# Kernel optimization log

Hardware: AMD Instinct MI355X
Metric: run time of the kernel (lower is better)

Reference implementation:

```python
import jax, jax.numpy as jnp
import numpy as np

# hyper_params (mode='test')
PRE_NMS = 1000
POST_NMS = 300
IOU_TH = 0.7
VARIANCES = np.array([0.1, 0.1, 0.2, 0.2], dtype=np.float32)
FM = 64            # feature map height/width
ANCHOR_COUNT = 9   # 3 scales x 3 ratios


def _make_anchors():
    """Normalized [y1,x1,y2,x2] anchors on a FM x FM grid, 9 per cell."""
    scales = np.array([0.1, 0.2, 0.4], np.float32)
    ratios = np.array([0.5, 1.0, 2.0], np.float32)
    ws = (scales[:, None] * np.sqrt(ratios)[None, :]).reshape(-1)  # (9,)
    hs = (scales[:, None] / np.sqrt(ratios)[None, :]).reshape(-1)  # (9,)
    ctr = (np.arange(FM, dtype=np.float32) + 0.5) / FM
    cy, cx = np.meshgrid(ctr, ctr, indexing='ij')                  # (FM,FM)
    cy = cy[..., None]; cx = cx[..., None]                         # (FM,FM,1)
    anchors = np.stack([cy - 0.5 * hs, cx - 0.5 * ws,
                        cy + 0.5 * hs, cx + 0.5 * ws], axis=-1)    # (FM,FM,9,4)
    return jnp.asarray(anchors.reshape(-1, 4))                     # (36864,4)


def setup_inputs() -> dict:
    key = jax.random.key(0)
    k1, k2 = jax.random.split(key)
    B = 16
    rpn_bbox_deltas = jax.random.normal(k1, (B, FM, FM, ANCHOR_COUNT * 4), dtype=jnp.float32)
    rpn_labels = jax.random.uniform(k2, (B, FM, FM, ANCHOR_COUNT), dtype=jnp.float32)
    return {"rpn_bbox_deltas": rpn_bbox_deltas,
            "rpn_labels": rpn_labels,
            "anchors": _make_anchors()}


def _nms_single(boxes):
    """Greedy NMS on score-sorted boxes (N,4) -> (POST_NMS,4), zero-padded."""
    N = boxes.shape[0]
    y1, x1, y2, x2 = boxes[:, 0], boxes[:, 1], boxes[:, 2], boxes[:, 3]
    area = (y2 - y1) * (x2 - x1)                                   # (N,)
    iy1 = jnp.maximum(y1[:, None], y1[None, :])
    ix1 = jnp.maximum(x1[:, None], x1[None, :])
    iy2 = jnp.minimum(y2[:, None], y2[None, :])
    ix2 = jnp.minimum(x2[:, None], x2[None, :])
    inter = jnp.maximum(iy2 - iy1, 0.0) * jnp.maximum(ix2 - ix1, 0.0)
    iou = inter / jnp.maximum(area[:, None] + area[None, :] - inter, 1e-9)  # (N,N)
    idx = jnp.arange(N)

    def body(i, keep):
        # if box i survives, suppress later boxes with high overlap
        suppress = keep[i] & (iou[i] > IOU_TH) & (idx > i)
        return keep & ~suppress

    keep = jax.lax.fori_loop(0, N, body, jnp.ones((N,), dtype=bool))
    # stable sort: kept boxes first, original (score-descending) order preserved
    order = jnp.argsort(jnp.where(keep, 0, 1))[:POST_NMS]
    sel = boxes[order]
    valid = keep[order]
    # combined_non_max_suppression clips output boxes to [0,1] and zero-pads
    return jnp.where(valid[:, None], jnp.clip(sel, 0.0, 1.0), 0.0)


def reference(rpn_bbox_deltas, rpn_labels, anchors):
    B = rpn_bbox_deltas.shape[0]
    N = anchors.shape[0]
    deltas = rpn_bbox_deltas.reshape(B, N, 4) * jnp.asarray(VARIANCES)
    labels = rpn_labels.reshape(B, N)

    # decode deltas against anchors
    anc_h = anchors[:, 2] - anchors[:, 0]
    anc_w = anchors[:, 3] - anchors[:, 1]
    anc_cy = anchors[:, 0] + 0.5 * anc_h
    anc_cx = anchors[:, 1] + 0.5 * anc_w
    h = jnp.exp(deltas[..., 2]) * anc_h
    w = jnp.exp(deltas[..., 3]) * anc_w
    cy = deltas[..., 0] * anc_h + anc_cy
    cx = deltas[..., 1] * anc_w + anc_cx
    boxes = jnp.stack([cy - 0.5 * h, cx - 0.5 * w,
                       cy + 0.5 * h, cx + 0.5 * w], axis=-1)       # (B,N,4)

    # top-k by objectness score (descending, so NMS input is pre-sorted)
    _, pre_idx = jax.lax.top_k(labels, PRE_NMS)                    # (B,PRE_NMS)
    pre_boxes = jnp.take_along_axis(boxes, pre_idx[..., None], axis=1)  # (B,PRE_NMS,4)

    roi_bboxes = jax.vmap(_nms_single)(pre_boxes)                  # (B,POST_NMS,4)
    return jax.lax.stop_gradient(roi_bboxes)
```

## Files before the change

kernel.cpp:

```cpp
#include <hip/hip_runtime.h>
#include <stdint.h>

#pragma clang fp contract(off)

#define N_ANCH 36864
#define PRE_NMS 1000
#define POST_NMS 300
#define SEL_CAP 1024
#define NWAVE 16

#define SLICES 16
#define K1_NT 256
#define SLICE_KEYS 2304
#define KEYS_PT 9
#define SLICE_TOP 128
#define COMPACT_CAP 192
#define MERGE_CAP 2048

#define NCOPY 8
#define HSTR 257

#define M_WSTRIDE 1024
#define M_WORDS_PER_B 16384
#define WS_BOX_FLOATS_PER_B 5120

#define K3_NT 512

__device__ __forceinline__ uint32_t mono_key(float v) {
    uint32_t u = __float_as_uint(v);
    return (u & 0x80000000u) ? ~u : (u | 0x80000000u);
}

__device__ __forceinline__ float clip01(float x) {
    return fminf(fmaxf(x, 0.0f), 1.0f);
}

__device__ __forceinline__ uint64_t bcast64(uint64_t v, int srclane) {
    uint32_t lo = (uint32_t)v, hi = (uint32_t)(v >> 32);
    lo = __builtin_amdgcn_readlane(lo, srclane);
    hi = __builtin_amdgcn_readlane(hi, srclane);
    return ((uint64_t)hi << 32) | (uint64_t)lo;
}

__device__ __forceinline__ uint64_t sfl64(uint64_t v) {
    uint32_t lo = __builtin_amdgcn_readfirstlane((uint32_t)v);
    uint32_t hi = __builtin_amdgcn_readfirstlane((uint32_t)(v >> 32));
    return ((uint64_t)hi << 32) | (uint64_t)lo;
}

__device__ __forceinline__ uint64_t bfly_or64(uint64_t v) {
    v |= __shfl_xor(v, 32);
    v |= __shfl_xor(v, 16);
    v |= __shfl_xor(v, 8);
    v |= __shfl_xor(v, 4);
    v |= __shfl_xor(v, 2);
    v |= __shfl_xor(v, 1);
    return v;
}

__device__ __forceinline__ void scan256(const uint32_t* __restrict__ h, uint32_t K,
                                        uint32_t* shm, uint32_t& outBin, uint32_t& outKrem) {
    const int t    = threadIdx.x;
    const int lane = t & 63;
    const int wv   = t >> 6;
    const uint32_t q = h[t];
    uint32_t sfx = q, o;
    o = __shfl_down(sfx, 1);  if (lane < 63) sfx += o;
    o = __shfl_down(sfx, 2);  if (lane < 62) sfx += o;
    o = __shfl_down(sfx, 4);  if (lane < 60) sfx += o;
    o = __shfl_down(sfx, 8);  if (lane < 56) sfx += o;
    o = __shfl_down(sfx, 16); if (lane < 48) sfx += o;
    o = __shfl_down(sfx, 32); if (lane < 32) sfx += o;
    if (lane == 0) shm[wv] = sfx;
    __syncthreads();
    uint32_t wAbove = 0;
    for (int w2 = wv + 1; w2 < 4; ++w2) wAbove += shm[w2];
    const uint32_t above = wAbove + (sfx - q);
    if ((above < K) && (above + q >= K)) { shm[4] = (uint32_t)t; shm[5] = K - above; }
    __syncthreads();
    outBin  = shm[4];
    outKrem = shm[5];
}

__global__ __launch_bounds__(K1_NT) void k1s_slice_top(
    const float* __restrict__ labels,
    uint64_t* __restrict__ wsCand)
{
    const int s = blockIdx.x;
    const int b = blockIdx.y;
    const int t = threadIdx.x;
    const int lane = t & 63;

    __shared__ uint32_t hc[NCOPY * HSTR];
    __shared__ uint32_t red[256];
    __shared__ uint32_t shm[8];
    __shared__ uint64_t cand[COMPACT_CAP];
    __shared__ uint32_t scnt;

    const float* lab = labels + (size_t)b * N_ANCH + (size_t)s * SLICE_KEYS;
    uint32_t key[KEYS_PT];
#pragma unroll
    for (int r = 0; r < KEYS_PT; ++r)
        key[r] = mono_key(lab[r * K1_NT + t]);

    for (int i = t; i < NCOPY * HSTR; i += K1_NT) hc[i] = 0u;
    if (t == 0) scnt = 0u;
    __syncthreads();

    const int cbase = (lane & 7) * HSTR;
#pragma unroll
    for (int r = 0; r < KEYS_PT; ++r)
        atomicAdd(&hc[cbase + (key[r] >> 24)], 1u);
    __syncthreads();
    uint32_t sum = 0;
#pragma unroll
    for (int c = 0; c < NCOPY; ++c) sum += hc[c * HSTR + t];
    red[t] = sum;
    __syncthreads();
    uint32_t b0, krem;
    scan256(red, SLICE_TOP, shm, b0, krem);
    __syncthreads();

    red[t] = 0u;
    __syncthreads();
#pragma unroll
    for (int r = 0; r < KEYS_PT; ++r)
        if ((key[r] >> 24) == b0) atomicAdd(&red[(key[r] >> 16) & 0xFFu], 1u);
    __syncthreads();
    uint32_t b1, krem2;
    scan256(red, krem, shm, b1, krem2);
    const uint32_t thresh16 = (b0 << 8) | b1;

#pragma unroll
    for (int r = 0; r < KEYS_PT; ++r) {
        const uint32_t u = key[r];
        const bool pred = (u >> 16) >= thresh16;
        const uint64_t bal = __ballot(pred ? 1 : 0);
        uint32_t base = 0;
        if (lane == 0 && bal)
            base = atomicAdd(&scnt, (uint32_t)__popcll(bal));
        base = __shfl(base, 0);
        if (pred) {
            const uint32_t off = (uint32_t)__popcll(bal & ((1ull << lane) - 1ull));
            const uint32_t pos = base + off;
            const uint32_t gi = (uint32_t)(s * SLICE_KEYS + r * K1_NT + t);
            if (pos < COMPACT_CAP)
                cand[pos] = ((uint64_t)u << 32) | (uint64_t)(0xFFFFFFFFu - gi);
        }
    }
    __syncthreads();
    uint32_t c = scnt; if (c > COMPACT_CAP) c = COMPACT_CAP;
    if (t >= (int)c && t < COMPACT_CAP) cand[t] = 0ull;
    __syncthreads();

    if (t < COMPACT_CAP) {
        const uint64_t mine = cand[t];
        uint32_t rank = 0;
        for (int i = 0; i < COMPACT_CAP; i += 4)
            rank += (cand[i]     > mine) + (cand[i + 1] > mine)
                  + (cand[i + 2] > mine) + (cand[i + 3] > mine);
        if (t < (int)c && rank < SLICE_TOP)
            wsCand[((size_t)b * SLICES + s) * SLICE_TOP + rank] = mine;
    }
}

__global__ __launch_bounds__(K1_NT) void k1m_merge_decode(
    const float* __restrict__ deltas,
    const float* __restrict__ anchors,
    const uint64_t* __restrict__ wsCand,
    float* __restrict__ wsBox)
{
    const int chunk = blockIdx.x;
    const int b     = blockIdx.y;
    const int t     = threadIdx.x;

    __shared__ uint64_t keyA[MERGE_CAP];
    const uint64_t* c2 = wsCand + (size_t)b * MERGE_CAP;
    for (int i = t; i < MERGE_CAP; i += K1_NT) keyA[i] = c2[i];
    __syncthreads();

    if (t < SLICE_TOP) {
        const uint64_t mine = keyA[chunk * SLICE_TOP + t];
        uint32_t lo[SLICES];
#pragma unroll
        for (int r = 0; r < SLICES; ++r) lo[r] = 0u;

#pragma unroll
        for (uint32_t s2 = 128; s2 > 0; s2 >>= 1) {
            uint64_t probe[SLICES];
#pragma unroll
            for (int r = 0; r < SLICES; ++r) {
                const uint32_t idx = lo[r] + s2 - 1u;
                probe[r] = keyA[r * SLICE_TOP + (idx < 128u ? idx : 0u)];
            }
#pragma unroll
            for (int r = 0; r < SLICES; ++r) {
                const uint32_t idx = lo[r] + s2 - 1u;
                if (idx < 128u && probe[r] > mine) lo[r] += s2;
            }
        }
        uint32_t rank = 0;
#pragma unroll
        for (int r = 0; r < SLICES; ++r) rank += lo[r];

        if (rank < PRE_NMS) {
            uint32_t idx = 0xFFFFFFFFu - (uint32_t)(mine & 0xFFFFFFFFull);
            float4 d4 = *(const float4*)(deltas + ((size_t)b * N_ANCH + idx) * 4);
            float4 a4 = *(const float4*)(anchors + (size_t)idx * 4);
            float anc_h  = a4.z - a4.x;
            float anc_w  = a4.w - a4.y;
            float anc_cy = a4.x + 0.5f * anc_h;
            float anc_cx = a4.y + 0.5f * anc_w;
            float dy = d4.x * 0.1f, dx = d4.y * 0.1f;
            float dh = d4.z * 0.2f, dw = d4.w * 0.2f;
            float h  = expf(dh) * anc_h;
            float w  = expf(dw) * anc_w;
            float cy = dy * anc_h + anc_cy;
            float cx = dx * anc_w + anc_cx;
            float y1 = cy - 0.5f * h, x1 = cx - 0.5f * w;
            float y2 = cy + 0.5f * h, x2 = cx + 0.5f * w;
            float* wb = wsBox + (size_t)b * WS_BOX_FLOATS_PER_B;
            wb[rank]              = y1;
            wb[SEL_CAP + rank]    = x1;
            wb[2*SEL_CAP + rank]  = y2;
            wb[3*SEL_CAP + rank]  = x2;
            wb[4*SEL_CAP + rank]  = (y2 - y1) * (x2 - x1);
        }
    }
}

__global__ __launch_bounds__(1024) void k2_iou_matrix(
    const float* __restrict__ wsBox,
    uint64_t* __restrict__ wsM)
{
    const int gx   = blockIdx.x;
    const int b    = blockIdx.y;
    const int t    = threadIdx.x;
    const int lane = t & 63;
    const int wave = t >> 6;

    int cb, r0, r1;
    if (gx < 16) { cb = gx;     r0 = 0;   r1 = 64 * (cb + 1); if (r1 > 512) r1 = 512; }
    else         { cb = gx - 8; r0 = 512; r1 = 64 * (cb + 1); }
    if (r1 > PRE_NMS) r1 = PRE_NMS;

    __shared__ float s[5 * SEL_CAP];
    const float4* b4 = (const float4*)(wsBox + (size_t)b * WS_BOX_FLOATS_PER_B);
    float4* s4 = (float4*)s;
    for (int i = t; i < (5 * SEL_CAP) / 4; i += 1024) s4[i] = b4[i];
    __syncthreads();

    float* ly1 = s;
    float* lx1 = s + SEL_CAP;
    float* ly2 = s + 2 * SEL_CAP;
    float* lx2 = s + 3 * SEL_CAP;
    float* lar = s + 4 * SEL_CAP;

    const int j = cb * 64 + lane;
    const float y1j = ly1[j], x1j = lx1[j], y2j = ly2[j], x2j = lx2[j], aj = lar[j];

    uint64_t* Mb = wsM + (size_t)b * M_WORDS_PER_B + (size_t)cb * M_WSTRIDE;
    for (int i = r0 + wave; i < r1; i += NWAVE) {
        float iy1 = fmaxf(ly1[i], y1j);
        float ix1 = fmaxf(lx1[i], x1j);
        float iy2 = fminf(ly2[i], y2j);
        float ix2 = fminf(lx2[i], x2j);
        float ih = iy2 - iy1; if (ih < 0.f) ih = 0.f;
        float iw = ix2 - ix1; if (iw < 0.f) iw = 0.f;
        float inter = ih * iw;
        float denom = lar[i] + aj - inter;
        if (denom < 1e-9f) denom = 1e-9f;
        float iou = inter / denom;
        bool sup = (j > i) && (iou > 0.7f);
        uint64_t mask = __ballot(sup ? 1 : 0);
        if (lane == 0) Mb[i] = mask;
    }
}

__global__ __launch_bounds__(K3_NT) void k3_reduce_out(
    const float* __restrict__ wsBox,
    const uint64_t* __restrict__ wsM,
    float* __restrict__ out)
{
    const int b    = blockIdx.x;
    const int t    = threadIdx.x;
    const int lane = t & 63;
    const int wave = t >> 6;

    __shared__ uint64_t remv[16];
    __shared__ uint64_t keepW[16];
    __shared__ uint32_t wordPref[16];

    const uint64_t* Mg = wsM + (size_t)b * M_WORDS_PER_B;

    if (t < 16) remv[t] = 0ull;

    uint64_t mDiag = 0ull, mSup = 0ull, selfC = 0ull;
    uint64_t mR1 = 0ull, mR2 = 0ull;
    if (wave == 0) {
        mDiag = Mg[lane];
        mSup  = Mg[(size_t)1 * M_WSTRIDE + lane];
    } else {
        mR1 = Mg[(size_t)(2 * wave)     * M_WSTRIDE + lane];
        mR2 = Mg[(size_t)(2 * wave + 1) * M_WSTRIDE + lane];
    }
    __syncthreads();

    for (int w = 0; w < 16; ++w) {
        if (wave == 0) {
            const uint64_t m  = mDiag;
            const uint64_t ms = mSup;
            if (w < 15) {
                mDiag = Mg[(size_t)(w + 1) * M_WSTRIDE + 64 * (w + 1) + lane];
                if (w < 14)
                    mSup = Mg[(size_t)(w + 2) * M_WSTRIDE + 64 * (w + 1) + lane];
            }
            const uint64_t valid = (w == 15) ? ((1ull << 40) - 1ull) : ~0ull;
            const bool laneValid = (w < 15) || (lane < 40);

            const uint64_t amS = sfl64(bfly_or64(laneValid ? m : 0ull));
            uint64_t cur = sfl64(remv[w] | selfC);

            const uint64_t Q        = amS & ~cur & valid;
            const uint64_t keptSure = valid & ~cur & ~Q;

            cur |= sfl64(bfly_or64(((keptSure >> lane) & 1ull) ? m : 0ull));

            uint64_t work = Q & ~cur;
            while (work) {
                const int bp = (int)__builtin_ctzll(work);
                cur |= bcast64(m, bp);
                work &= ~(1ull << bp);
                work &= ~cur;
            }

            const uint64_t keep = (~cur) & valid;
            if (lane == 0) keepW[w] = keep;
            if (w < 15)
                selfC = bfly_or64(((keep >> lane) & 1ull) ? ms : 0ull);
        } else if (w >= 1) {
            const int v1 = 2 * wave, v2 = 2 * wave + 1;
            const uint64_t a1 = mR1, a2 = mR2;
            if (v1 >= w + 2) mR1 = Mg[(size_t)v1 * M_WSTRIDE + 64 * w + lane];
            if (v2 >= w + 2) mR2 = Mg[(size_t)v2 * M_WSTRIDE + 64 * w + lane];
            const uint64_t km = keepW[w - 1];
            if (v1 >= w + 1) {
                uint64_t x = ((km >> lane) & 1ull) ? a1 : 0ull;
                x = bfly_or64(x);
                if (lane == 0) remv[v1] |= x;
            }
            if (v2 >= w + 1) {
                uint64_t x = ((km >> lane) & 1ull) ? a2 : 0ull;
                x = bfly_or64(x);
                if (lane == 0) remv[v2] |= x;
            }
        }
        __syncthreads();
    }

    if (t == 0) {
        uint32_t acc = 0u;
        for (int w = 0; w < 16; ++w) {
            wordPref[w] = acc;
            acc += (uint32_t)__popcll(keepW[w]);
        }
    }
    float* ob = out + (size_t)b * (POST_NMS * 4);
    for (int i = t; i < POST_NMS * 4; i += K3_NT) ob[i] = 0.0f;
    __syncthreads();

    for (int tt = t; tt < PRE_NMS; tt += K3_NT) {
        const int w = tt >> 6, bpos = tt & 63;
        uint64_t kw = keepW[w];
        if ((kw >> bpos) & 1ull) {
            uint32_t rank = wordPref[w] +
                            (uint32_t)__popcll(kw & ((1ull << bpos) - 1ull));
            if (rank < POST_NMS) {
                const float* wb = wsBox + (size_t)b * WS_BOX_FLOATS_PER_B;
                float* o = ob + (size_t)rank * 4;
                o[0] = clip01(wb[tt]);
                o[1] = clip01(wb[SEL_CAP + tt]);
                o[2] = clip01(wb[2*SEL_CAP + tt]);
                o[3] = clip01(wb[3*SEL_CAP + tt]);
            }
        }
    }
}

extern "C" void kernel_launch(void* const* d_in, const int* in_sizes, int n_in,
                              void* d_out, int out_size, void* d_ws, size_t ws_size,
                              hipStream_t stream) {
    const float* deltas  = (const float*)d_in[0];
    const float* labels  = (const float*)d_in[1];
    const float* anchors = (const float*)d_in[2];
    float* out = (float*)d_out;
    const int B = in_sizes[1] / N_ANCH;

    char* p = (char*)d_ws;
    uint64_t* wsCand = (uint64_t*)p;
    float*    wsBox  = (float*)(p + (size_t)B * MERGE_CAP * 8);
    uint64_t* wsM    = (uint64_t*)(p + (size_t)B * MERGE_CAP * 8
                                     + (size_t)B * WS_BOX_FLOATS_PER_B * 4);

    k1s_slice_top<<<dim3(SLICES, B), K1_NT, 0, stream>>>(labels, wsCand);
    k1m_merge_decode<<<dim3(SLICES, B), K1_NT, 0, stream>>>(deltas, anchors, wsCand, wsBox);
    k2_iou_matrix<<<dim3(24, B), 1024, 0, stream>>>(wsBox, wsM);
    k3_reduce_out<<<B, K3_NT, 0, stream>>>(wsBox, wsM, out);
}
```

Baseline: 108.8 us.

## Process NMS mask words in pairs to halve barrier rounds, trim slice-top syncs

The bitmask NMS reduction now handles two 64-box words per barrier round. Wave 0 resolves both diagonal blocks and carries the cross-pair suppression through bridge registers, so the loop runs 8 rounds instead of 16. The helper waves each fold two kept words per round. In the slice top-k kernel, a second histogram buffer removes two barriers and a clear pass, and the merge kernel loads candidates with 16-byte vector copies. The cost is more registers and more serial work for wave 0 in each round.

```diff
diff --git a/kernel.cpp b/kernel.cpp
--- a/kernel.cpp
+++ b/kernel.cpp
@@ -93,6 +93,7 @@
 
     __shared__ uint32_t hc[NCOPY * HSTR];
     __shared__ uint32_t red[256];
+    __shared__ uint32_t red2[256];
     __shared__ uint32_t shm[8];
     __shared__ uint64_t cand[COMPACT_CAP];
     __shared__ uint32_t scnt;
@@ -104,6 +105,7 @@
         key[r] = mono_key(lab[r * K1_NT + t]);
 
     for (int i = t; i < NCOPY * HSTR; i += K1_NT) hc[i] = 0u;
+    red2[t] = 0u;
     if (t == 0) scnt = 0u;
     __syncthreads();
 
@@ -116,19 +118,15 @@
 #pragma unroll
     for (int c = 0; c < NCOPY; ++c) sum += hc[c * HSTR + t];
     red[t] = sum;
-    __syncthreads();
     uint32_t b0, krem;
     scan256(red, SLICE_TOP, shm, b0, krem);
-    __syncthreads();
-
-    red[t] = 0u;
-    __syncthreads();
+
 #pragma unroll
     for (int r = 0; r < KEYS_PT; ++r)
-        if ((key[r] >> 24) == b0) atomicAdd(&red[(key[r] >> 16) & 0xFFu], 1u);
+        if ((key[r] >> 24) == b0) atomicAdd(&red2[(key[r] >> 16) & 0xFFu], 1u);
     __syncthreads();
     uint32_t b1, krem2;
-    scan256(red, krem, shm, b1, krem2);
+    scan256(red2, krem, shm, b1, krem2);
     const uint32_t thresh16 = (b0 << 8) | b1;
 
 #pragma unroll
@@ -174,9 +172,11 @@
     const int b     = blockIdx.y;
     const int t     = threadIdx.x;
 
-    __shared__ uint64_t keyA[MERGE_CAP];
-    const uint64_t* c2 = wsCand + (size_t)b * MERGE_CAP;
-    for (int i = t; i < MERGE_CAP; i += K1_NT) keyA[i] = c2[i];
+    __shared__ __align__(16) uint64_t keyA[MERGE_CAP];
+    const uint4* c4 = (const uint4*)(wsCand + (size_t)b * MERGE_CAP);
+    uint4* k4 = (uint4*)keyA;
+#pragma unroll
+    for (int i = t; i < MERGE_CAP / 2; i += K1_NT) k4[i] = c4[i];
     __syncthreads();
 
     if (t < SLICE_TOP) {
@@ -295,65 +295,102 @@
 
     if (t < 16) remv[t] = 0ull;
 
-    uint64_t mDiag = 0ull, mSup = 0ull, selfC = 0ull;
-    uint64_t mR1 = 0ull, mR2 = 0ull;
+    uint64_t dA = 0, dB = 0, sAB = 0, brA2 = 0, brB2 = 0, brA3 = 0, brB3 = 0;
+    uint64_t mA1 = 0, mB1 = 0, mA2 = 0, mB2 = 0;
     if (wave == 0) {
-        mDiag = Mg[lane];
-        mSup  = Mg[(size_t)1 * M_WSTRIDE + lane];
-    } else {
-        mR1 = Mg[(size_t)(2 * wave)     * M_WSTRIDE + lane];
-        mR2 = Mg[(size_t)(2 * wave + 1) * M_WSTRIDE + lane];
-    }
-    __syncthreads();
-
-    for (int w = 0; w < 16; ++w) {
+        dA   = Mg[lane];
+        dB   = Mg[(size_t)1 * M_WSTRIDE + 64 + lane];
+        sAB  = Mg[(size_t)1 * M_WSTRIDE + lane];
+        brA2 = Mg[(size_t)2 * M_WSTRIDE + lane];
+        brB2 = Mg[(size_t)2 * M_WSTRIDE + 64 + lane];
+        brA3 = Mg[(size_t)3 * M_WSTRIDE + lane];
+        brB3 = Mg[(size_t)3 * M_WSTRIDE + 64 + lane];
+    } else if (wave <= 6) {
+        const int v1 = 2 * wave + 2, v2 = 2 * wave + 3;
+        mA1 = Mg[(size_t)v1 * M_WSTRIDE + lane];
+        mB1 = Mg[(size_t)v1 * M_WSTRIDE + 64 + lane];
+        mA2 = Mg[(size_t)v2 * M_WSTRIDE + lane];
+        mB2 = Mg[(size_t)v2 * M_WSTRIDE + 64 + lane];
+    }
+    uint64_t bridgeA = 0ull, bridgeB = 0ull;
+    __syncthreads();
+
+    for (int p = 0; p < 8; ++p) {
         if (wave == 0) {
-            const uint64_t m  = mDiag;
-            const uint64_t ms = mSup;
-            if (w < 15) {
-                mDiag = Mg[(size_t)(w + 1) * M_WSTRIDE + 64 * (w + 1) + lane];
-                if (w < 14)
-                    mSup = Mg[(size_t)(w + 2) * M_WSTRIDE + 64 * (w + 1) + lane];
-            }
-            const uint64_t valid = (w == 15) ? ((1ull << 40) - 1ull) : ~0ull;
-            const bool laneValid = (w < 15) || (lane < 40);
-
-            const uint64_t amS = sfl64(bfly_or64(laneValid ? m : 0ull));
-            uint64_t cur = sfl64(remv[w] | selfC);
-
-            const uint64_t Q        = amS & ~cur & valid;
-            const uint64_t keptSure = valid & ~cur & ~Q;
-
-            cur |= sfl64(bfly_or64(((keptSure >> lane) & 1ull) ? m : 0ull));
-
-            uint64_t work = Q & ~cur;
-            while (work) {
-                const int bp = (int)__builtin_ctzll(work);
-                cur |= bcast64(m, bp);
-                work &= ~(1ull << bp);
-                work &= ~cur;
-            }
-
-            const uint64_t keep = (~cur) & valid;
-            if (lane == 0) keepW[w] = keep;
-            if (w < 15)
-                selfC = bfly_or64(((keep >> lane) & 1ull) ? ms : 0ull);
-        } else if (w >= 1) {
-            const int v1 = 2 * wave, v2 = 2 * wave + 1;
-            const uint64_t a1 = mR1, a2 = mR2;
-            if (v1 >= w + 2) mR1 = Mg[(size_t)v1 * M_WSTRIDE + 64 * w + lane];
-            if (v2 >= w + 2) mR2 = Mg[(size_t)v2 * M_WSTRIDE + 64 * w + lane];
-            const uint64_t km = keepW[w - 1];
-            if (v1 >= w + 1) {
-                uint64_t x = ((km >> lane) & 1ull) ? a1 : 0ull;
-                x = bfly_or64(x);
-                if (lane == 0) remv[v1] |= x;
-            }
-            if (v2 >= w + 1) {
-                uint64_t x = ((km >> lane) & 1ull) ? a2 : 0ull;
-                x = bfly_or64(x);
-                if (lane == 0) remv[v2] |= x;
-            }
+            const int a = 2 * p, bw = 2 * p + 1;
+            const uint64_t mda = dA, mdb = dB, msab = sAB;
+            const uint64_t b2a = brA2, b2b = brB2, b3a = brA3, b3b = brB3;
+            if (p < 7) {
+                const int an = 2 * p + 2, bn = 2 * p + 3;
+                dA  = Mg[(size_t)an * M_WSTRIDE + 64 * an + lane];
+                dB  = Mg[(size_t)bn * M_WSTRIDE + 64 * bn + lane];
+                sAB = Mg[(size_t)bn * M_WSTRIDE + 64 * an + lane];
+                if (p < 6) {
+                    const int a3 = 2 * p + 4, b3 = 2 * p + 5;
+                    brA2 = Mg[(size_t)a3 * M_WSTRIDE + 64 * an + lane];
+                    brB2 = Mg[(size_t)a3 * M_WSTRIDE + 64 * bn + lane];
+                    brA3 = Mg[(size_t)b3 * M_WSTRIDE + 64 * an + lane];
+                    brB3 = Mg[(size_t)b3 * M_WSTRIDE + 64 * bn + lane];
+                }
+            }
+            uint64_t curA = sfl64(remv[a]) | sfl64(bridgeA);
+            {
+                const uint64_t amS = sfl64(bfly_or64(mda));
+                const uint64_t Q        = amS & ~curA;
+                const uint64_t keptSure = ~curA & ~Q;
+                curA |= sfl64(bfly_or64(((keptSure >> lane) & 1ull) ? mda : 0ull));
+                uint64_t work = Q & ~curA;
+                while (work) {
+                    const int bp = (int)__builtin_ctzll(work);
+                    curA |= bcast64(mda, bp);
+                    work &= ~(1ull << bp);
+                    work &= ~curA;
+                }
+            }
+            const uint64_t keepA = ~curA;
+            const uint64_t sc = bfly_or64(((keepA >> lane) & 1ull) ? msab : 0ull);
+            const uint64_t validB = (bw == 15) ? ((1ull << 40) - 1ull) : ~0ull;
+            uint64_t curB = sfl64(remv[bw]) | sfl64(bridgeB) | sfl64(sc);
+            {
+                const bool lv = (bw < 15) || (lane < 40);
+                const uint64_t amS = sfl64(bfly_or64(lv ? mdb : 0ull));
+                const uint64_t Q        = amS & ~curB & validB;
+                const uint64_t keptSure = validB & ~curB & ~Q;
+                curB |= sfl64(bfly_or64(((keptSure >> lane) & 1ull) ? mdb : 0ull));
+                uint64_t work = Q & ~curB;
+                while (work) {
+                    const int bp = (int)__builtin_ctzll(work);
+                    curB |= bcast64(mdb, bp);
+                    work &= ~(1ull << bp);
+                    work &= ~curB;
+                }
+            }
+            const uint64_t keepB = (~curB) & validB;
+            if (lane == 0) { keepW[a] = keepA; keepW[bw] = keepB; }
+            if (p < 7) {
+                bridgeA = bfly_or64((((keepA >> lane) & 1ull) ? b2a : 0ull) |
+                                    (((keepB >> lane) & 1ull) ? b2b : 0ull));
+                bridgeB = bfly_or64((((keepA >> lane) & 1ull) ? b3a : 0ull) |
+                                    (((keepB >> lane) & 1ull) ? b3b : 0ull));
+            }
+        } else if (wave <= 6 && p >= 1 && p <= wave) {
+            const int v1 = 2 * wave + 2, v2 = 2 * wave + 3;
+            const uint64_t a1 = mA1, b1 = mB1, a2 = mA2, b2 = mB2;
+            if (p < wave) {
+                mA1 = Mg[(size_t)v1 * M_WSTRIDE + 64 * (2 * p)     + lane];
+                mB1 = Mg[(size_t)v1 * M_WSTRIDE + 64 * (2 * p + 1) + lane];
+                mA2 = Mg[(size_t)v2 * M_WSTRIDE + 64 * (2 * p)     + lane];
+                mB2 = Mg[(size_t)v2 * M_WSTRIDE + 64 * (2 * p + 1) + lane];
+            }
+            const uint64_t kmA = keepW[2 * p - 2];
+            const uint64_t kmB = keepW[2 * p - 1];
+            uint64_t x1 = (((kmA >> lane) & 1ull) ? a1 : 0ull) |
+                          (((kmB >> lane) & 1ull) ? b1 : 0ull);
+            x1 = bfly_or64(x1);
+            uint64_t x2 = (((kmA >> lane) & 1ull) ? a2 : 0ull) |
+                          (((kmB >> lane) & 1ull) ? b2 : 0ull);
+            x2 = bfly_or64(x2);
+            if (lane == 0) { remv[v1] |= x1; remv[v2] |= x2; }
         }
         __syncthreads();
     }
```

After: 106.7 us. Within noise of the previous version (-2.0%).
